# Performance work log

Measured on AMD Instinct MI355X. Metric: run time of the kernel, lower is better.

## Reference

```python
import jax, jax.numpy as jnp
import numpy as np

# TensorProductConvLayer (DiffDock-style): gather -> edge-MLP-weighted fully
# connected tensor product (lmax=1 irreps) -> scatter-mean.
# in/out irreps: ns x0e + nv x1o + nv x1e + ns x0o ; sh irreps: 1x0e + 1x1o
NS, NV = 16, 4
N_NODES, N_EDGES = 8000, 160000
EDGE_FEAT = 3 * NS                      # 48
IRREPS_DIM = 2 * NS + 6 * NV            # 56
# per-path weight block sizes (fully-connected 'uvw' paths, mul2 = 1):
# [A:0e*0e->0e, B:1o*1o->0e, A:0e*1o->1o, B:1o*0e->1o, C:1e*1o->1o,
#  B:1o*1o->1e, C:1e*0e->1e, D:0o*1o->1e, C:1e*1o->0o, D:0o*0e->0o]
PATH_SIZES = [NS*NS, NV*NS, NS*NV, NV*NV, NV*NV, NV*NV, NV*NV, NS*NV, NV*NS, NS*NS]
W_NUMEL = sum(PATH_SIZES)               # 832
# component-normalized CG factors: 1x1->0 uses delta/sqrt(3); 1x1->1 uses eps/sqrt(2)
INV_SQRT3 = float(1.0 / np.sqrt(3.0))
INV_SQRT2 = float(1.0 / np.sqrt(2.0))
# element path normalization: 1/sqrt(total fan-in mul per output irrep)
A_SCAL = float(1.0 / np.sqrt(NS + NV))      # 0e / 0o outputs
A_VEC = float(1.0 / np.sqrt(NS + 2 * NV))   # 1o / 1e outputs


def setup_inputs() -> dict:
    key = jax.random.key(0)
    ks = jax.random.split(key, 6)
    node_attr = jax.random.normal(ks[0], (N_NODES, IRREPS_DIM), jnp.float32)
    edge_index = jax.random.randint(ks[1], (2, N_EDGES), 0, N_NODES)
    edge_attr = jax.random.normal(ks[2], (N_EDGES, EDGE_FEAT), jnp.float32)
    edge_sh = jax.random.normal(ks[3], (N_EDGES, 4), jnp.float32)
    s = float(1.0 / np.sqrt(EDGE_FEAT))
    fc_w1 = jax.random.normal(ks[4], (EDGE_FEAT, EDGE_FEAT), jnp.float32) * s
    fc_b1 = jnp.zeros((EDGE_FEAT,), jnp.float32)
    fc_w2 = jax.random.normal(ks[5], (EDGE_FEAT, W_NUMEL), jnp.float32) * s
    fc_b2 = jnp.zeros((W_NUMEL,), jnp.float32)
    return dict(node_attr=node_attr, edge_attr=edge_attr, edge_sh=edge_sh,
                fc_w1=fc_w1, fc_b1=fc_b1, fc_w2=fc_w2, fc_b2=fc_b2,
                edge_index=edge_index)


def _split_weights(w):
    outs, off = [], 0
    for sz in PATH_SIZES:
        outs.append(w[:, off:off + sz])
        off += sz
    return outs


def _tp_conv(node_attr, edge_attr, edge_sh, fc_w1, fc_b1, fc_w2, fc_b2, src, dst):
    # edge MLP -> per-edge tensor-product weights [E, 832]
    h = jax.nn.relu(edge_attr @ fc_w1 + fc_b1)
    w = h @ fc_w2 + fc_b2
    wA0, wB0, wA1, wB1, wC1, wB1e, wC1e, wD1e, wC0o, wD0o = _split_weights(w)

    x = node_attr[dst]                         # gather [E, 56]
    x0e = x[:, :NS]
    x1o = x[:, NS:NS + 3 * NV].reshape(-1, NV, 3)
    x1e = x[:, NS + 3 * NV:NS + 6 * NV].reshape(-1, NV, 3)
    x0o = x[:, NS + 6 * NV:]
    s0 = edge_sh[:, 0]
    s1 = edge_sh[:, 1:4]

    # ---- 0e output [E, ns]
    o0e = jnp.einsum('eu,euv->ev', x0e, wA0.reshape(-1, NS, NS)) * s0[:, None]
    dot_b = jnp.einsum('eui,ei->eu', x1o, s1) * INV_SQRT3   # 1o x 1o -> 0e
    o0e = (o0e + jnp.einsum('eu,euv->ev', dot_b, wB0.reshape(-1, NV, NS))) * A_SCAL

    # ---- 1o output [E, nv, 3]
    o1o = jnp.einsum('eu,euv->ev', x0e, wA1.reshape(-1, NS, NV))[:, :, None] * s1[:, None, :]
    o1o = o1o + jnp.einsum('eui,euv->evi', x1o, wB1.reshape(-1, NV, NV)) * s0[:, None, None]
    cr_e = jnp.cross(x1e, s1[:, None, :]) * INV_SQRT2       # 1e x 1o -> 1o
    o1o = (o1o + jnp.einsum('eui,euv->evi', cr_e, wC1.reshape(-1, NV, NV))) * A_VEC

    # ---- 1e output [E, nv, 3]
    cr_o = jnp.cross(x1o, s1[:, None, :]) * INV_SQRT2       # 1o x 1o -> 1e
    o1e = jnp.einsum('eui,euv->evi', cr_o, wB1e.reshape(-1, NV, NV))
    o1e = o1e + jnp.einsum('eui,euv->evi', x1e, wC1e.reshape(-1, NV, NV)) * s0[:, None, None]
    o1e = (o1e + jnp.einsum('eu,euv->ev', x0o, wD1e.reshape(-1, NS, NV))[:, :, None] * s1[:, None, :]) * A_VEC

    # ---- 0o output [E, ns]
    dot_c = jnp.einsum('eui,ei->eu', x1e, s1) * INV_SQRT3   # 1e x 1o -> 0o
    o0o = jnp.einsum('eu,euv->ev', dot_c, wC0o.reshape(-1, NV, NS))
    o0o = (o0o + jnp.einsum('eu,euv->ev', x0o, wD0o.reshape(-1, NS, NS)) * s0[:, None]) * A_SCAL

    tp = jnp.concatenate([o0e, o1o.reshape(-1, 3 * NV), o1e.reshape(-1, 3 * NV), o0o], axis=-1)

    # scatter-mean over source nodes
    summed = jax.ops.segment_sum(tp, src, num_segments=N_NODES)
    counts = jax.ops.segment_sum(jnp.ones((tp.shape[0],), tp.dtype), src, num_segments=N_NODES)
    return summed / jnp.maximum(counts, 1.0)[:, None]


def reference(node_attr, edge_attr, edge_sh, fc_w1, fc_b1, fc_w2, fc_b2, edge_index):
    src, dst = edge_index[0], edge_index[1]
    return _tp_conv(node_attr, edge_attr, edge_sh, fc_w1, fc_b1, fc_w2, fc_b2, src, dst)
```

## Files before the change

### kernel.cpp

```cpp
#include <hip/hip_runtime.h>
#include <hip/hip_fp16.h>

#define IRR    56
#define EF     48
#define WN     832
#define NEDGE  160000
#define NNODE  8000
#define NT     256
#define TE2    64
#define NTASK  (NEDGE / TE2)
#define GRID   512

#define INV_SQRT3 0.5773502691896258f
#define INV_SQRT2 0.7071067811865476f
#define A_SCAL    0.22360679774997896f
#define A_VEC     0.20412414523193154f

typedef __bf16 bf16x8 __attribute__((ext_vector_type(8)));
typedef float  f32x4  __attribute__((ext_vector_type(4)));
typedef unsigned short u16x8 __attribute__((ext_vector_type(8)));
typedef unsigned short u16x4 __attribute__((ext_vector_type(4)));

__device__ __forceinline__ unsigned short f2bf(float f) {
    unsigned int u = __builtin_bit_cast(unsigned int, f);
    u += 0x7FFFu + ((u >> 16) & 1u);
    return (unsigned short)(u >> 16);
}
__device__ __forceinline__ unsigned short f2h(float f) {
    __half h = __float2half(f);
    return __builtin_bit_cast(unsigned short, h);
}
__device__ __forceinline__ float h2f(unsigned short u) {
    __half h = __builtin_bit_cast(__half, u);
    return __half2float(h);
}

__global__ void k_setup(const float* __restrict__ w1, const float* __restrict__ b1,
                        const float* __restrict__ w2, const float* __restrict__ b2,
                        unsigned short* __restrict__ W1T, unsigned short* __restrict__ W2L,
                        const int* __restrict__ edge_index, int* __restrict__ hist)
{
    int o = blockIdx.x * 256 + threadIdx.x;
    if (o < 52 * 2 * 64 * 8) {
        int i = o >> 10;
        int rem = o & 1023;
        int f = rem >> 9;
        int rem2 = rem & 511;
        int l = rem2 >> 3, j = rem2 & 7;
        int mm = l & 15, qq = l >> 4;
        int k = f * 32 + qq * 8 + j;
        int n = i * 16 + mm;
        float v = (k < EF) ? w2[k * WN + n] : ((k == EF) ? b2[n] : 0.f);
        W2L[o] = f2bf(v);
    }
    if (o < EF * EF) { int k = o / EF, n = o - k * EF; W1T[n * 64 + k] = f2bf(w1[o]); }
    if (o < EF * 16) { int n = o >> 4, kk = EF + (o & 15); W1T[n * 64 + kk] = (kk == EF) ? f2bf(b1[n]) : (unsigned short)0; }
    if (o < NEDGE) atomicAdd(&hist[edge_index[o]], 1);
}

__global__ __launch_bounds__(NT, 2) void tp_fused(
    const float* __restrict__ node_attr,
    const float* __restrict__ edge_attr,
    const float* __restrict__ edge_sh,
    const int*   __restrict__ edge_index,
    const int*   __restrict__ hist,
    const unsigned short* __restrict__ W1T,
    const unsigned short* __restrict__ W2L,
    float* __restrict__ out)
{
    __shared__ __align__(16) unsigned short sW2[26 * 1024];
    __shared__ __align__(16) unsigned char  UGH[TE2 * 56 * 4];
    __shared__ __align__(16) unsigned char  UFO[TE2 * 60 * 2];
    __shared__ float sS1[TE2][4];
    __shared__ int   sSrc[TE2], sDst[TE2];
    __shared__ float sInv[TE2];

    float*          sG   = (float*)UGH;
    unsigned short* sH   = (unsigned short*)UGH;
    unsigned short* sF16 = (unsigned short*)UFO;
    float*          sO   = (float*)UFO;

    const int tid    = threadIdx.x;
    const int lane   = tid & 63;
    const int wv     = tid >> 6;
    const int m      = lane & 15;
    const int quad   = lane >> 4;
    const int em     = wv * 16 + m;
    const int flavor = blockIdx.x & 1;
    const int bid2   = blockIdx.x >> 1;

    {
        const uint4* src = (const uint4*)(W2L + (size_t)flavor * 26 * 1024);
        uint4* dst = (uint4*)sW2;
        #pragma unroll
        for (int it = 0; it < 13; it++) dst[it * NT + tid] = src[it * NT + tid];
    }

    for (int task = bid2; task < NTASK; task += 256) {
        const int e0 = task * TE2;
        __syncthreads();
        if (tid < TE2)            sSrc[tid]       = edge_index[e0 + tid];
        else if (tid < 2 * TE2)   sDst[tid - TE2] = edge_index[NEDGE + e0 + tid - TE2];
        __syncthreads();

        {
            const float* nrow = node_attr + (size_t)sDst[em] * IRR;
            float* g = sG + em * 56;
            #pragma unroll
            for (int t = 0; t < 3; t++) {
                int c = quad + t * 4;
                *(float4*)(g + c * 4) = *(const float4*)(nrow + c * 4);
            }
            if (quad < 2) { int c = 12 + quad; *(float4*)(g + c * 4) = *(const float4*)(nrow + c * 4); }
        }
        if (tid >= 128 && tid < 128 + TE2) {
            int e = tid - 128;
            sInv[e] = 1.0f / fmaxf((float)hist[sSrc[e]], 1.0f);
        }
        __syncthreads();

        if (quad == 0) {
            const float* x = sG + em * 56;
            float4 sh4 = *(const float4*)&edge_sh[(size_t)(e0 + em) * 4];
            const float s0 = sh4.x, sx = sh4.y, sy = sh4.z, sz = sh4.w;
            unsigned short* F = sF16 + em * 60;
            const float c0S = s0 * A_SCAL;
            const float c0V = s0 * A_VEC;
            const float cD3 = INV_SQRT3 * A_SCAL;
            const float cC2 = INV_SQRT2 * A_VEC;
            if (flavor == 0) {
                #pragma unroll
                for (int u = 0; u < 16; u++) {
                    float x0e = x[u];
                    F[u]      = f2h(x0e * c0S);
                    F[20 + u] = f2h(x0e * A_VEC);
                }
                #pragma unroll
                for (int u = 0; u < 4; u++) {
                    float a0 = x[16 + u*3], a1 = x[16 + u*3 + 1], a2 = x[16 + u*3 + 2];
                    float b0 = x[28 + u*3], b1 = x[28 + u*3 + 1], b2 = x[28 + u*3 + 2];
                    F[16 + u] = f2h((a0*sx + a1*sy + a2*sz) * cD3);
                    F[36 + u*3 + 0] = f2h(a0 * c0V);
                    F[36 + u*3 + 1] = f2h(a1 * c0V);
                    F[36 + u*3 + 2] = f2h(a2 * c0V);
                    F[48 + u*3 + 0] = f2h((b1*sz - b2*sy) * cC2);
                    F[48 + u*3 + 1] = f2h((b2*sx - b0*sz) * cC2);
                    F[48 + u*3 + 2] = f2h((b0*sy - b1*sx) * cC2);
                }
            } else {
                #pragma unroll
                for (int u = 0; u < 4; u++) {
                    float a0 = x[16 + u*3], a1 = x[16 + u*3 + 1], a2 = x[16 + u*3 + 2];
                    float b0 = x[28 + u*3], b1 = x[28 + u*3 + 1], b2 = x[28 + u*3 + 2];
                    F[u*3 + 0]      = f2h((a1*sz - a2*sy) * cC2);
                    F[u*3 + 1]      = f2h((a2*sx - a0*sz) * cC2);
                    F[u*3 + 2]      = f2h((a0*sy - a1*sx) * cC2);
                    F[12 + u*3 + 0] = f2h(b0 * c0V);
                    F[12 + u*3 + 1] = f2h(b1 * c0V);
                    F[12 + u*3 + 2] = f2h(b2 * c0V);
                    F[40 + u]       = f2h((b0*sx + b1*sy + b2*sz) * cD3);
                }
                #pragma unroll
                for (int u = 0; u < 16; u++) {
                    float x0o = x[40 + u];
                    F[24 + u] = f2h(x0o * A_VEC);
                    F[44 + u] = f2h(x0o * c0S);
                }
            }
            sS1[em][0] = sx; sS1[em][1] = sy; sS1[em][2] = sz;
        }
        __syncthreads();

        {
            const float* arow = edge_attr + (size_t)(e0 + em) * EF;
            float av0[8], av1[8];
            {
                float4 p0 = *(const float4*)(arow + quad * 8);
                float4 p1 = *(const float4*)(arow + quad * 8 + 4);
                av0[0]=p0.x; av0[1]=p0.y; av0[2]=p0.z; av0[3]=p0.w;
                av0[4]=p1.x; av0[5]=p1.y; av0[6]=p1.z; av0[7]=p1.w;
            }
            if (quad < 2) {
                float4 p0 = *(const float4*)(arow + 32 + quad * 8);
                float4 p1 = *(const float4*)(arow + 32 + quad * 8 + 4);
                av1[0]=p0.x; av1[1]=p0.y; av1[2]=p0.z; av1[3]=p0.w;
                av1[4]=p1.x; av1[5]=p1.y; av1[6]=p1.z; av1[7]=p1.w;
            } else {
                #pragma unroll
                for (int j = 0; j < 8; j++) av1[j] = 0.f;
                if (quad == 2) av1[0] = 1.f;
            }
            u16x8 ub0, ub1;
            #pragma unroll
            for (int j = 0; j < 8; j++) { ub0[j] = f2bf(av0[j]); ub1[j] = f2bf(av1[j]); }
            bf16x8 hb0 = __builtin_bit_cast(bf16x8, ub0);
            bf16x8 hb1 = __builtin_bit_cast(bf16x8, ub1);

            #pragma unroll
            for (int nth = 0; nth < 3; nth++) {
                bf16x8 a0 = __builtin_bit_cast(bf16x8, *(const u16x8*)&W1T[(nth*16 + m)*64 + quad*8]);
                bf16x8 a1 = __builtin_bit_cast(bf16x8, *(const u16x8*)&W1T[(nth*16 + m)*64 + 32 + quad*8]);
                f32x4 c = {0.f, 0.f, 0.f, 0.f};
                c = __builtin_amdgcn_mfma_f32_16x16x32_bf16(a0, hb0, c, 0, 0, 0);
                c = __builtin_amdgcn_mfma_f32_16x16x32_bf16(a1, hb1, c, 0, 0, 0);
                u16x4 hp;
                #pragma unroll
                for (int r = 0; r < 4; r++) hp[r] = f2bf(fmaxf(c[r], 0.f));
                *(u16x4*)&sH[em * 72 + nth*16 + quad*4] = hp;
            }
            if (quad == 3) {
                u16x4 b = {0x3F80, 0, 0, 0}, z = {0, 0, 0, 0};
                *(u16x4*)&sH[em * 72 + 48] = b;
                *(u16x4*)&sH[em * 72 + 52] = z;
                *(u16x4*)&sH[em * 72 + 56] = z;
                *(u16x4*)&sH[em * 72 + 60] = z;
            }
        }
        __syncthreads();

        bf16x8 HB0 = __builtin_bit_cast(bf16x8, *(const u16x8*)&sH[em * 72 + quad*8]);
        bf16x8 HB1 = __builtin_bit_cast(bf16x8, *(const u16x8*)&sH[em * 72 + 32 + quad*8]);

        const unsigned short* Fp = sF16 + em * 60;
        const float s1x = sS1[em][0], s1y = sS1[em][1], s1z = sS1[em][2];

        if (flavor == 0) {
            float oe[4] = {0.f,0.f,0.f,0.f};
            float sA[4] = {0.f,0.f,0.f,0.f};
            float t1[12] = {0.f,0.f,0.f,0.f,0.f,0.f,0.f,0.f,0.f,0.f,0.f,0.f};
            #pragma unroll
            for (int i = 0; i < 26; i++) {
                u16x8 Af = *(const u16x8*)&sW2[i * 1024 + lane * 8];
                u16x8 Bf = *(const u16x8*)&sW2[i * 1024 + 512 + lane * 8];
                f32x4 c = {0.f,0.f,0.f,0.f};
                c = __builtin_amdgcn_mfma_f32_16x16x32_bf16(__builtin_bit_cast(bf16x8, Af), HB0, c, 0, 0, 0);
                c = __builtin_amdgcn_mfma_f32_16x16x32_bf16(__builtin_bit_cast(bf16x8, Bf), HB1, c, 0, 0, 0);
                if (i < 20) {
                    float f = h2f(Fp[i]);
                    #pragma unroll
                    for (int r = 0; r < 4; r++) oe[r] += f * c[r];
                } else if (i < 24) {
                    float f = h2f(Fp[20 + (i - 20)*4 + quad]);
                    #pragma unroll
                    for (int r = 0; r < 4; r++) sA[r] += f * c[r];
                } else {
                    int u = (i - 24)*4 + quad;
                    #pragma unroll
                    for (int i3 = 0; i3 < 3; i3++) {
                        float f = h2f(Fp[36 + u*3 + i3]);
                        #pragma unroll
                        for (int r = 0; r < 4; r++) t1[i3*4 + r] += f * c[r];
                    }
                }
            }
            #pragma unroll
            for (int r = 0; r < 4; r++) {
                sA[r] += __shfl_xor(sA[r], 16, 64);  sA[r] += __shfl_xor(sA[r], 32, 64);
            }
            #pragma unroll
            for (int i = 0; i < 12; i++) {
                t1[i] += __shfl_xor(t1[i], 16, 64);  t1[i] += __shfl_xor(t1[i], 32, 64);
            }
            __syncthreads();
            float4 v0; v0.x = oe[0]; v0.y = oe[1]; v0.z = oe[2]; v0.w = oe[3];
            *(float4*)&sO[em * 28 + quad*4] = v0;
            if (quad == 0) {
                #pragma unroll
                for (int r = 0; r < 4; r++) {
                    sO[em * 28 + 16 + r*3 + 0] = sA[r] * s1x + t1[0*4 + r];
                    sO[em * 28 + 16 + r*3 + 1] = sA[r] * s1y + t1[1*4 + r];
                    sO[em * 28 + 16 + r*3 + 2] = sA[r] * s1z + t1[2*4 + r];
                }
            }
        } else {
            float sD[4] = {0.f,0.f,0.f,0.f};
            float t1[12] = {0.f,0.f,0.f,0.f,0.f,0.f,0.f,0.f,0.f,0.f,0.f,0.f};
            float oo[4] = {0.f,0.f,0.f,0.f};
            #pragma unroll
            for (int i = 0; i < 26; i++) {
                u16x8 Af = *(const u16x8*)&sW2[i * 1024 + lane * 8];
                u16x8 Bf = *(const u16x8*)&sW2[i * 1024 + 512 + lane * 8];
                f32x4 c = {0.f,0.f,0.f,0.f};
                c = __builtin_amdgcn_mfma_f32_16x16x32_bf16(__builtin_bit_cast(bf16x8, Af), HB0, c, 0, 0, 0);
                c = __builtin_amdgcn_mfma_f32_16x16x32_bf16(__builtin_bit_cast(bf16x8, Bf), HB1, c, 0, 0, 0);
                if (i < 2) {
                    int j = i*4 + quad;
                    #pragma unroll
                    for (int i3 = 0; i3 < 3; i3++) {
                        float f = h2f(Fp[j*3 + i3]);
                        #pragma unroll
                        for (int r = 0; r < 4; r++) t1[i3*4 + r] += f * c[r];
                    }
                } else if (i < 6) {
                    float f = h2f(Fp[24 + (i - 2)*4 + quad]);
                    #pragma unroll
                    for (int r = 0; r < 4; r++) sD[r] += f * c[r];
                } else {
                    float f = h2f(Fp[40 + (i - 6)]);
                    #pragma unroll
                    for (int r = 0; r < 4; r++) oo[r] += f * c[r];
                }
            }
            #pragma unroll
            for (int r = 0; r < 4; r++) {
                sD[r] += __shfl_xor(sD[r], 16, 64);  sD[r] += __shfl_xor(sD[r], 32, 64);
            }
            #pragma unroll
            for (int i = 0; i < 12; i++) {
                t1[i] += __shfl_xor(t1[i], 16, 64);  t1[i] += __shfl_xor(t1[i], 32, 64);
            }
            __syncthreads();
            float4 v1; v1.x = oo[0]; v1.y = oo[1]; v1.z = oo[2]; v1.w = oo[3];
            *(float4*)&sO[em * 28 + 12 + quad*4] = v1;
            if (quad == 0) {
                #pragma unroll
                for (int r = 0; r < 4; r++) {
                    sO[em * 28 + r*3 + 0] = sD[r] * s1x + t1[0*4 + r];
                    sO[em * 28 + r*3 + 1] = sD[r] * s1y + t1[1*4 + r];
                    sO[em * 28 + r*3 + 2] = sD[r] * s1z + t1[2*4 + r];
                }
            }
        }
        __syncthreads();

        #pragma unroll
        for (int it = 0; it < 7; it++) {
            int idx = it * NT + tid;
            int e = idx / 28, ch = idx - e * 28;
            unsafeAtomicAdd(&out[(size_t)sSrc[e] * IRR + flavor * 28 + ch],
                            sO[e * 28 + ch] * sInv[e]);
        }
    }
}

extern "C" void kernel_launch(void* const* d_in, const int* in_sizes, int n_in,
                              void* d_out, int out_size, void* d_ws, size_t ws_size,
                              hipStream_t stream) {
    const float* node_attr  = (const float*)d_in[0];
    const float* edge_attr  = (const float*)d_in[1];
    const float* edge_sh    = (const float*)d_in[2];
    const float* fc_w1      = (const float*)d_in[3];
    const float* fc_b1      = (const float*)d_in[4];
    const float* fc_w2      = (const float*)d_in[5];
    const float* fc_b2      = (const float*)d_in[6];
    const int*   edge_index = (const int*)d_in[7];

    int* hist = (int*)d_ws;
    unsigned short* W1T = (unsigned short*)(hist + NNODE);
    unsigned short* W2L = W1T + EF * 64;

    hipMemsetAsync(hist, 0, NNODE * sizeof(int), stream);
    hipMemsetAsync(d_out, 0, (size_t)out_size * sizeof(float), stream);

    k_setup<<<(NEDGE + 255) / 256, 256, 0, stream>>>(
        fc_w1, fc_b1, fc_w2, fc_b2, W1T, W2L, edge_index, hist);

    tp_fused<<<GRID, NT, 0, stream>>>(node_attr, edge_attr, edge_sh, edge_index,
                                      hist, W1T, W2L, (float*)d_out);
}
```

Before: 177.9 us.

## Drop persistent LDS-resident W2 loop for one-block-per-tile grid with global weight reads

Replaces the persistent kernel, which staged the second-layer weights into about 52KB of shared memory per block, with a grid of one block per 64-edge tile per flavor. The weights are now read straight from global memory and served from cache, and launch bounds rise to 4 blocks per CU. The per-edge factor computation is spread across all four quads and stored as fp32 instead of fp16. Several barriers per tile are removed. The aim is more occupancy and less synchronization, at the cost of repeated global or L2 weight fetches per MFMA and more blocks to launch.

```diff
diff --git a/kernel.cpp b/kernel.cpp
--- a/kernel.cpp
+++ b/kernel.cpp
@@ -9,7 +9,7 @@
 #define NT     256
 #define TE2    64
 #define NTASK  (NEDGE / TE2)
-#define GRID   512
+#define GRID   (2 * NTASK)
 
 #define INV_SQRT3 0.5773502691896258f
 #define INV_SQRT2 0.7071067811865476f
@@ -25,14 +25,6 @@
     unsigned int u = __builtin_bit_cast(unsigned int, f);
     u += 0x7FFFu + ((u >> 16) & 1u);
     return (unsigned short)(u >> 16);
-}
-__device__ __forceinline__ unsigned short f2h(float f) {
-    __half h = __float2half(f);
-    return __builtin_bit_cast(unsigned short, h);
-}
-__device__ __forceinline__ float h2f(unsigned short u) {
-    __half h = __builtin_bit_cast(__half, u);
-    return __half2float(h);
 }
 
 __global__ void k_setup(const float* __restrict__ w1, const float* __restrict__ b1,
@@ -58,7 +50,7 @@
     if (o < NEDGE) atomicAdd(&hist[edge_index[o]], 1);
 }
 
-__global__ __launch_bounds__(NT, 2) void tp_fused(
+__global__ __launch_bounds__(NT, 4) void tp_fused(
     const float* __restrict__ node_attr,
     const float* __restrict__ edge_attr,
     const float* __restrict__ edge_sh,
@@ -68,17 +60,14 @@
     const unsigned short* __restrict__ W2L,
     float* __restrict__ out)
 {
-    __shared__ __align__(16) unsigned short sW2[26 * 1024];
-    __shared__ __align__(16) unsigned char  UGH[TE2 * 56 * 4];
-    __shared__ __align__(16) unsigned char  UFO[TE2 * 60 * 2];
-    __shared__ float sS1[TE2][4];
+    __shared__ __align__(16) unsigned char UGH[TE2 * 56 * 4];
+    __shared__ __align__(16) float sF[TE2 * 61];
+    __shared__ __align__(16) float sO[TE2 * 28];
     __shared__ int   sSrc[TE2], sDst[TE2];
     __shared__ float sInv[TE2];
 
-    float*          sG   = (float*)UGH;
-    unsigned short* sH   = (unsigned short*)UGH;
-    unsigned short* sF16 = (unsigned short*)UFO;
-    float*          sO   = (float*)UFO;
+    float*          sG = (float*)UGH;
+    unsigned short* sH = (unsigned short*)UGH;
 
     const int tid    = threadIdx.x;
     const int lane   = tid & 63;
@@ -87,249 +76,239 @@
     const int quad   = lane >> 4;
     const int em     = wv * 16 + m;
     const int flavor = blockIdx.x & 1;
-    const int bid2   = blockIdx.x >> 1;
+    const int e0     = (blockIdx.x >> 1) * TE2;
+
+    if (tid < TE2)            sSrc[tid]       = edge_index[e0 + tid];
+    else if (tid < 2 * TE2)   sDst[tid - TE2] = edge_index[NEDGE + e0 + tid - TE2];
+    __syncthreads();
 
     {
-        const uint4* src = (const uint4*)(W2L + (size_t)flavor * 26 * 1024);
-        uint4* dst = (uint4*)sW2;
-        #pragma unroll
-        for (int it = 0; it < 13; it++) dst[it * NT + tid] = src[it * NT + tid];
-    }
-
-    for (int task = bid2; task < NTASK; task += 256) {
-        const int e0 = task * TE2;
-        __syncthreads();
-        if (tid < TE2)            sSrc[tid]       = edge_index[e0 + tid];
-        else if (tid < 2 * TE2)   sDst[tid - TE2] = edge_index[NEDGE + e0 + tid - TE2];
-        __syncthreads();
-
+        const float* nrow = node_attr + (size_t)sDst[em] * IRR;
+        float* g = sG + em * 56;
+        #pragma unroll
+        for (int t = 0; t < 3; t++) {
+            int c = quad + t * 4;
+            *(float4*)(g + c * 4) = *(const float4*)(nrow + c * 4);
+        }
+        if (quad < 2) { int c = 12 + quad; *(float4*)(g + c * 4) = *(const float4*)(nrow + c * 4); }
+    }
+    if (tid >= 128 && tid < 128 + TE2) {
+        int e = tid - 128;
+        sInv[e] = 1.0f / fmaxf((float)hist[sSrc[e]], 1.0f);
+    }
+
+    float4 sh4 = *(const float4*)&edge_sh[(size_t)(e0 + em) * 4];
+    const float s0 = sh4.x, sx = sh4.y, sy = sh4.z, sz = sh4.w;
+
+    {
+        const float* x = sG + em * 56;
+        float* F = sF + em * 61;
+        const float c0S = s0 * A_SCAL;
+        const float c0V = s0 * A_VEC;
+        const float cD3 = INV_SQRT3 * A_SCAL;
+        const float cC2 = INV_SQRT2 * A_VEC;
+        if (flavor == 0) {
+            #pragma unroll
+            for (int t = 0; t < 4; t++) {
+                int u = quad * 4 + t;
+                float x0e = x[u];
+                F[u]      = x0e * c0S;
+                F[20 + u] = x0e * A_VEC;
+            }
+            {
+                int u = quad;
+                float a0 = x[16 + u*3], a1 = x[16 + u*3 + 1], a2 = x[16 + u*3 + 2];
+                float b0 = x[28 + u*3], b1 = x[28 + u*3 + 1], b2 = x[28 + u*3 + 2];
+                F[16 + u] = (a0*sx + a1*sy + a2*sz) * cD3;
+                F[36 + u*3 + 0] = a0 * c0V;
+                F[36 + u*3 + 1] = a1 * c0V;
+                F[36 + u*3 + 2] = a2 * c0V;
+                F[48 + u*3 + 0] = (b1*sz - b2*sy) * cC2;
+                F[48 + u*3 + 1] = (b2*sx - b0*sz) * cC2;
+                F[48 + u*3 + 2] = (b0*sy - b1*sx) * cC2;
+            }
+        } else {
+            {
+                int u = quad;
+                float a0 = x[16 + u*3], a1 = x[16 + u*3 + 1], a2 = x[16 + u*3 + 2];
+                float b0 = x[28 + u*3], b1 = x[28 + u*3 + 1], b2 = x[28 + u*3 + 2];
+                F[u*3 + 0]      = (a1*sz - a2*sy) * cC2;
+                F[u*3 + 1]      = (a2*sx - a0*sz) * cC2;
+                F[u*3 + 2]      = (a0*sy - a1*sx) * cC2;
+                F[12 + u*3 + 0] = b0 * c0V;
+                F[12 + u*3 + 1] = b1 * c0V;
+                F[12 + u*3 + 2] = b2 * c0V;
+                F[40 + u]       = (b0*sx + b1*sy + b2*sz) * cD3;
+            }
+            #pragma unroll
+            for (int t = 0; t < 4; t++) {
+                int u = quad * 4 + t;
+                float x0o = x[40 + u];
+                F[24 + u] = x0o * A_VEC;
+                F[44 + u] = x0o * c0S;
+            }
+        }
+    }
+
+    bf16x8 hb0, hb1;
+    {
+        const float* arow = edge_attr + (size_t)(e0 + em) * EF;
+        float av0[8], av1[8];
         {
-            const float* nrow = node_attr + (size_t)sDst[em] * IRR;
-            float* g = sG + em * 56;
-            #pragma unroll
-            for (int t = 0; t < 3; t++) {
-                int c = quad + t * 4;
-                *(float4*)(g + c * 4) = *(const float4*)(nrow + c * 4);
-            }
-            if (quad < 2) { int c = 12 + quad; *(float4*)(g + c * 4) = *(const float4*)(nrow + c * 4); }
-        }
-        if (tid >= 128 && tid < 128 + TE2) {
-            int e = tid - 128;
-            sInv[e] = 1.0f / fmaxf((float)hist[sSrc[e]], 1.0f);
-        }
-        __syncthreads();
-
+            float4 p0 = *(const float4*)(arow + quad * 8);
+            float4 p1 = *(const float4*)(arow + quad * 8 + 4);
+            av0[0]=p0.x; av0[1]=p0.y; av0[2]=p0.z; av0[3]=p0.w;
+            av0[4]=p1.x; av0[5]=p1.y; av0[6]=p1.z; av0[7]=p1.w;
+        }
+        if (quad < 2) {
+            float4 p0 = *(const float4*)(arow + 32 + quad * 8);
+            float4 p1 = *(const float4*)(arow + 32 + quad * 8 + 4);
+            av1[0]=p0.x; av1[1]=p0.y; av1[2]=p0.z; av1[3]=p0.w;
+            av1[4]=p1.x; av1[5]=p1.y; av1[6]=p1.z; av1[7]=p1.w;
+        } else {
+            #pragma unroll
+            for (int j = 0; j < 8; j++) av1[j] = 0.f;
+            if (quad == 2) av1[0] = 1.f;
+        }
+        u16x8 ub0, ub1;
+        #pragma unroll
+        for (int j = 0; j < 8; j++) { ub0[j] = f2bf(av0[j]); ub1[j] = f2bf(av1[j]); }
+        hb0 = __builtin_bit_cast(bf16x8, ub0);
+        hb1 = __builtin_bit_cast(bf16x8, ub1);
+    }
+
+    __syncthreads();
+
+    #pragma unroll
+    for (int nth = 0; nth < 3; nth++) {
+        bf16x8 a0 = __builtin_bit_cast(bf16x8, *(const u16x8*)&W1T[(nth*16 + m)*64 + quad*8]);
+        bf16x8 a1 = __builtin_bit_cast(bf16x8, *(const u16x8*)&W1T[(nth*16 + m)*64 + 32 + quad*8]);
+        f32x4 c = {0.f, 0.f, 0.f, 0.f};
+        c = __builtin_amdgcn_mfma_f32_16x16x32_bf16(a0, hb0, c, 0, 0, 0);
+        c = __builtin_amdgcn_mfma_f32_16x16x32_bf16(a1, hb1, c, 0, 0, 0);
+        u16x4 hp;
+        #pragma unroll
+        for (int r = 0; r < 4; r++) hp[r] = f2bf(fmaxf(c[r], 0.f));
+        *(u16x4*)&sH[em * 72 + nth*16 + quad*4] = hp;
+    }
+    if (quad == 3) {
+        u16x4 b = {0x3F80, 0, 0, 0}, z = {0, 0, 0, 0};
+        *(u16x4*)&sH[em * 72 + 48] = b;
+        *(u16x4*)&sH[em * 72 + 52] = z;
+        *(u16x4*)&sH[em * 72 + 56] = z;
+        *(u16x4*)&sH[em * 72 + 60] = z;
+    }
+
+    bf16x8 HB0 = __builtin_bit_cast(bf16x8, *(const u16x8*)&sH[em * 72 + quad*8]);
+    bf16x8 HB1 = __builtin_bit_cast(bf16x8, *(const u16x8*)&sH[em * 72 + 32 + quad*8]);
+
+    const float* Fp = sF + em * 61;
+    const unsigned short* Wt = W2L + (size_t)flavor * 26 * 1024;
+
+    if (flavor == 0) {
+        float oe[4] = {0.f,0.f,0.f,0.f};
+        float sA[4] = {0.f,0.f,0.f,0.f};
+        float t1[12] = {0.f,0.f,0.f,0.f,0.f,0.f,0.f,0.f,0.f,0.f,0.f,0.f};
+        #pragma unroll
+        for (int i = 0; i < 26; i++) {
+            u16x8 Af = *(const u16x8*)&Wt[i * 1024 + lane * 8];
+            u16x8 Bf = *(const u16x8*)&Wt[i * 1024 + 512 + lane * 8];
+            f32x4 c = {0.f,0.f,0.f,0.f};
+            c = __builtin_amdgcn_mfma_f32_16x16x32_bf16(__builtin_bit_cast(bf16x8, Af), HB0, c, 0, 0, 0);
+            c = __builtin_amdgcn_mfma_f32_16x16x32_bf16(__builtin_bit_cast(bf16x8, Bf), HB1, c, 0, 0, 0);
+            if (i < 20) {
+                float f = Fp[i];
+                #pragma unroll
+                for (int r = 0; r < 4; r++) oe[r] += f * c[r];
+            } else if (i < 24) {
+                float f = Fp[20 + (i - 20)*4 + quad];
+                #pragma unroll
+                for (int r = 0; r < 4; r++) sA[r] += f * c[r];
+            } else {
+                int u = (i - 24)*4 + quad;
+                #pragma unroll
+                for (int i3 = 0; i3 < 3; i3++) {
+                    float f = Fp[36 + u*3 + i3];
+                    #pragma unroll
+                    for (int r = 0; r < 4; r++) t1[i3*4 + r] += f * c[r];
+                }
+            }
+        }
+        #pragma unroll
+        for (int r = 0; r < 4; r++) {
+            sA[r] += __shfl_xor(sA[r], 16, 64);  sA[r] += __shfl_xor(sA[r], 32, 64);
+        }
+        #pragma unroll
+        for (int i = 0; i < 12; i++) {
+            t1[i] += __shfl_xor(t1[i], 16, 64);  t1[i] += __shfl_xor(t1[i], 32, 64);
+        }
+        float4 v0; v0.x = oe[0]; v0.y = oe[1]; v0.z = oe[2]; v0.w = oe[3];
+        *(float4*)&sO[em * 28 + quad*4] = v0;
         if (quad == 0) {
-            const float* x = sG + em * 56;
-            float4 sh4 = *(const float4*)&edge_sh[(size_t)(e0 + em) * 4];
-            const float s0 = sh4.x, sx = sh4.y, sy = sh4.z, sz = sh4.w;
-            unsigned short* F = sF16 + em * 60;
-            const float c0S = s0 * A_SCAL;
-            const float c0V = s0 * A_VEC;
-            const float cD3 = INV_SQRT3 * A_SCAL;
-            const float cC2 = INV_SQRT2 * A_VEC;
-            if (flavor == 0) {
-                #pragma unroll
-                for (int u = 0; u < 16; u++) {
-                    float x0e = x[u];
-                    F[u]      = f2h(x0e * c0S);
-                    F[20 + u] = f2h(x0e * A_VEC);
+            #pragma unroll
+            for (int r = 0; r < 4; r++) {
+                sO[em * 28 + 16 + r*3 + 0] = sA[r] * sx + t1[0*4 + r];
+                sO[em * 28 + 16 + r*3 + 1] = sA[r] * sy + t1[1*4 + r];
+                sO[em * 28 + 16 + r*3 + 2] = sA[r] * sz + t1[2*4 + r];
+            }
+        }
+    } else {
+        float sD[4] = {0.f,0.f,0.f,0.f};
+        float t1[12] = {0.f,0.f,0.f,0.f,0.f,0.f,0.f,0.f,0.f,0.f,0.f,0.f};
+        float oo[4] = {0.f,0.f,0.f,0.f};
+        #pragma unroll
+        for (int i = 0; i < 26; i++) {
+            u16x8 Af = *(const u16x8*)&Wt[i * 1024 + lane * 8];
+            u16x8 Bf = *(const u16x8*)&Wt[i * 1024 + 512 + lane * 8];
+            f32x4 c = {0.f,0.f,0.f,0.f};
+            c = __builtin_amdgcn_mfma_f32_16x16x32_bf16(__builtin_bit_cast(bf16x8, Af), HB0, c, 0, 0, 0);
+            c = __builtin_amdgcn_mfma_f32_16x16x32_bf16(__builtin_bit_cast(bf16x8, Bf), HB1, c, 0, 0, 0);
+            if (i < 2) {
+                int j = i*4 + quad;
+                #pragma unroll
+                for (int i3 = 0; i3 < 3; i3++) {
+                    float f = Fp[j*3 + i3];
+                    #pragma unroll
+                    for (int r = 0; r < 4; r++) t1[i3*4 + r] += f * c[r];
                 }
-                #pragma unroll
-                for (int u = 0; u < 4; u++) {
-                    float a0 = x[16 + u*3], a1 = x[16 + u*3 + 1], a2 = x[16 + u*3 + 2];
-                    float b0 = x[28 + u*3], b1 = x[28 + u*3 + 1], b2 = x[28 + u*3 + 2];
-                    F[16 + u] = f2h((a0*sx + a1*sy + a2*sz) * cD3);
-                    F[36 + u*3 + 0] = f2h(a0 * c0V);
-                    F[36 + u*3 + 1] = f2h(a1 * c0V);
-                    F[36 + u*3 + 2] = f2h(a2 * c0V);
-                    F[48 + u*3 + 0] = f2h((b1*sz - b2*sy) * cC2);
-                    F[48 + u*3 + 1] = f2h((b2*sx - b0*sz) * cC2);
-                    F[48 + u*3 + 2] = f2h((b0*sy - b1*sx) * cC2);
-                }
+            } else if (i < 6) {
+                float f = Fp[24 + (i - 2)*4 + quad];
+                #pragma unroll
+                for (int r = 0; r < 4; r++) sD[r] += f * c[r];
             } else {
-                #pragma unroll
-                for (int u = 0; u < 4; u++) {
-                    float a0 = x[16 + u*3], a1 = x[16 + u*3 + 1], a2 = x[16 + u*3 + 2];
-                    float b0 = x[28 + u*3], b1 = x[28 + u*3 + 1], b2 = x[28 + u*3 + 2];
-                    F[u*3 + 0]      = f2h((a1*sz - a2*sy) * cC2);
-                    F[u*3 + 1]      = f2h((a2*sx - a0*sz) * cC2);
-                    F[u*3 + 2]      = f2h((a0*sy - a1*sx) * cC2);
-                    F[12 + u*3 + 0] = f2h(b0 * c0V);
-                    F[12 + u*3 + 1] = f2h(b1 * c0V);
-                    F[12 + u*3 + 2] = f2h(b2 * c0V);
-                    F[40 + u]       = f2h((b0*sx + b1*sy + b2*sz) * cD3);
-                }
-                #pragma unroll
-                for (int u = 0; u < 16; u++) {
-                    float x0o = x[40 + u];
-                    F[24 + u] = f2h(x0o * A_VEC);
-                    F[44 + u] = f2h(x0o * c0S);
-                }
-            }
-            sS1[em][0] = sx; sS1[em][1] = sy; sS1[em][2] = sz;
-        }
-        __syncthreads();
-
-        {
-            const float* arow = edge_attr + (size_t)(e0 + em) * EF;
-            float av0[8], av1[8];
-            {
-                float4 p0 = *(const float4*)(arow + quad * 8);
-                float4 p1 = *(const float4*)(arow + quad * 8 + 4);
-                av0[0]=p0.x; av0[1]=p0.y; av0[2]=p0.z; av0[3]=p0.w;
-                av0[4]=p1.x; av0[5]=p1.y; av0[6]=p1.z; av0[7]=p1.w;
-            }
-            if (quad < 2) {
-                float4 p0 = *(const float4*)(arow + 32 + quad * 8);
-                float4 p1 = *(const float4*)(arow + 32 + quad * 8 + 4);
-                av1[0]=p0.x; av1[1]=p0.y; av1[2]=p0.z; av1[3]=p0.w;
-                av1[4]=p1.x; av1[5]=p1.y; av1[6]=p1.z; av1[7]=p1.w;
-            } else {
-                #pragma unroll
-                for (int j = 0; j < 8; j++) av1[j] = 0.f;
-                if (quad == 2) av1[0] = 1.f;
-            }
-            u16x8 ub0, ub1;
-            #pragma unroll
-            for (int j = 0; j < 8; j++) { ub0[j] = f2bf(av0[j]); ub1[j] = f2bf(av1[j]); }
-            bf16x8 hb0 = __builtin_bit_cast(bf16x8, ub0);
-            bf16x8 hb1 = __builtin_bit_cast(bf16x8, ub1);
-
-            #pragma unroll
-            for (int nth = 0; nth < 3; nth++) {
-                bf16x8 a0 = __builtin_bit_cast(bf16x8, *(const u16x8*)&W1T[(nth*16 + m)*64 + quad*8]);
-                bf16x8 a1 = __builtin_bit_cast(bf16x8, *(const u16x8*)&W1T[(nth*16 + m)*64 + 32 + quad*8]);
-                f32x4 c = {0.f, 0.f, 0.f, 0.f};
-                c = __builtin_amdgcn_mfma_f32_16x16x32_bf16(a0, hb0, c, 0, 0, 0);
-                c = __builtin_amdgcn_mfma_f32_16x16x32_bf16(a1, hb1, c, 0, 0, 0);
-                u16x4 hp;
-                #pragma unroll
-                for (int r = 0; r < 4; r++) hp[r] = f2bf(fmaxf(c[r], 0.f));
-                *(u16x4*)&sH[em * 72 + nth*16 + quad*4] = hp;
-            }
-            if (quad == 3) {
-                u16x4 b = {0x3F80, 0, 0, 0}, z = {0, 0, 0, 0};
-                *(u16x4*)&sH[em * 72 + 48] = b;
-                *(u16x4*)&sH[em * 72 + 52] = z;
-                *(u16x4*)&sH[em * 72 + 56] = z;
-                *(u16x4*)&sH[em * 72 + 60] = z;
-            }
-        }
-        __syncthreads();
-
-        bf16x8 HB0 = __builtin_bit_cast(bf16x8, *(const u16x8*)&sH[em * 72 + quad*8]);
-        bf16x8 HB1 = __builtin_bit_cast(bf16x8, *(const u16x8*)&sH[em * 72 + 32 + quad*8]);
-
-        const unsigned short* Fp = sF16 + em * 60;
-        const float s1x = sS1[em][0], s1y = sS1[em][1], s1z = sS1[em][2];
-
-        if (flavor == 0) {
-            float oe[4] = {0.f,0.f,0.f,0.f};
-            float sA[4] = {0.f,0.f,0.f,0.f};
-            float t1[12] = {0.f,0.f,0.f,0.f,0.f,0.f,0.f,0.f,0.f,0.f,0.f,0.f};
-            #pragma unroll
-            for (int i = 0; i < 26; i++) {
-                u16x8 Af = *(const u16x8*)&sW2[i * 1024 + lane * 8];
-                u16x8 Bf = *(const u16x8*)&sW2[i * 1024 + 512 + lane * 8];
-                f32x4 c = {0.f,0.f,0.f,0.f};
-                c = __builtin_amdgcn_mfma_f32_16x16x32_bf16(__builtin_bit_cast(bf16x8, Af), HB0, c, 0, 0, 0);
-                c = __builtin_amdgcn_mfma_f32_16x16x32_bf16(__builtin_bit_cast(bf16x8, Bf), HB1, c, 0, 0, 0);
-                if (i < 20) {
-                    float f = h2f(Fp[i]);
-                    #pragma unroll
-                    for (int r = 0; r < 4; r++) oe[r] += f * c[r];
-                } else if (i < 24) {
-                    float f = h2f(Fp[20 + (i - 20)*4 + quad]);
-                    #pragma unroll
-                    for (int r = 0; r < 4; r++) sA[r] += f * c[r];
-                } else {
-                    int u = (i - 24)*4 + quad;
-                    #pragma unroll
-                    for (int i3 = 0; i3 < 3; i3++) {
-                        float f = h2f(Fp[36 + u*3 + i3]);
-                        #pragma unroll
-                        for (int r = 0; r < 4; r++) t1[i3*4 + r] += f * c[r];
-                    }
-                }
-            }
+                float f = Fp[40 + (i - 6)];
+                #pragma unroll
+                for (int r = 0; r < 4; r++) oo[r] += f * c[r];
+            }
+        }
+        #pragma unroll
+        for (int r = 0; r < 4; r++) {
+            sD[r] += __shfl_xor(sD[r], 16, 64);  sD[r] += __shfl_xor(sD[r], 32, 64);
+        }
+        #pragma unroll
+        for (int i = 0; i < 12; i++) {
+            t1[i] += __shfl_xor(t1[i], 16, 64);  t1[i] += __shfl_xor(t1[i], 32, 64);
+        }
+        float4 v1; v1.x = oo[0]; v1.y = oo[1]; v1.z = oo[2]; v1.w = oo[3];
+        *(float4*)&sO[em * 28 + 12 + quad*4] = v1;
+        if (quad == 0) {
             #pragma unroll
             for (int r = 0; r < 4; r++) {
-                sA[r] += __shfl_xor(sA[r], 16, 64);  sA[r] += __shfl_xor(sA[r], 32, 64);
-            }
-            #pragma unroll
-            for (int i = 0; i < 12; i++) {
-                t1[i] += __shfl_xor(t1[i], 16, 64);  t1[i] += __shfl_xor(t1[i], 32, 64);
-            }
-            __syncthreads();
-            float4 v0; v0.x = oe[0]; v0.y = oe[1]; v0.z = oe[2]; v0.w = oe[3];
-            *(float4*)&sO[em * 28 + quad*4] = v0;
-            if (quad == 0) {
-                #pragma unroll
-                for (int r = 0; r < 4; r++) {
-                    sO[em * 28 + 16 + r*3 + 0] = sA[r] * s1x + t1[0*4 + r];
-                    sO[em * 28 + 16 + r*3 + 1] = sA[r] * s1y + t1[1*4 + r];
-                    sO[em * 28 + 16 + r*3 + 2] = sA[r] * s1z + t1[2*4 + r];
-                }
-            }
-        } else {
-            float sD[4] = {0.f,0.f,0.f,0.f};
-            float t1[12] = {0.f,0.f,0.f,0.f,0.f,0.f,0.f,0.f,0.f,0.f,0.f,0.f};
-            float oo[4] = {0.f,0.f,0.f,0.f};
-            #pragma unroll
-            for (int i = 0; i < 26; i++) {
-                u16x8 Af = *(const u16x8*)&sW2[i * 1024 + lane * 8];
-                u16x8 Bf = *(const u16x8*)&sW2[i * 1024 + 512 + lane * 8];
-                f32x4 c = {0.f,0.f,0.f,0.f};
-                c = __builtin_amdgcn_mfma_f32_16x16x32_bf16(__builtin_bit_cast(bf16x8, Af), HB0, c, 0, 0, 0);
-                c = __builtin_amdgcn_mfma_f32_16x16x32_bf16(__builtin_bit_cast(bf16x8, Bf), HB1, c, 0, 0, 0);
-                if (i < 2) {
-                    int j = i*4 + quad;
-                    #pragma unroll
-                    for (int i3 = 0; i3 < 3; i3++) {
-                        float f = h2f(Fp[j*3 + i3]);
-                        #pragma unroll
-                        for (int r = 0; r < 4; r++) t1[i3*4 + r] += f * c[r];
-                    }
-                } else if (i < 6) {
-                    float f = h2f(Fp[24 + (i - 2)*4 + quad]);
-                    #pragma unroll
-                    for (int r = 0; r < 4; r++) sD[r] += f * c[r];
-                } else {
-                    float f = h2f(Fp[40 + (i - 6)]);
-                    #pragma unroll
-                    for (int r = 0; r < 4; r++) oo[r] += f * c[r];
-                }
-            }
-            #pragma unroll
-            for (int r = 0; r < 4; r++) {
-                sD[r] += __shfl_xor(sD[r], 16, 64);  sD[r] += __shfl_xor(sD[r], 32, 64);
-            }
-            #pragma unroll
-            for (int i = 0; i < 12; i++) {
-                t1[i] += __shfl_xor(t1[i], 16, 64);  t1[i] += __shfl_xor(t1[i], 32, 64);
-            }
-            __syncthreads();
-            float4 v1; v1.x = oo[0]; v1.y = oo[1]; v1.z = oo[2]; v1.w = oo[3];
-            *(float4*)&sO[em * 28 + 12 + quad*4] = v1;
-            if (quad == 0) {
-                #pragma unroll
-                for (int r = 0; r < 4; r++) {
-                    sO[em * 28 + r*3 + 0] = sD[r] * s1x + t1[0*4 + r];
-                    sO[em * 28 + r*3 + 1] = sD[r] * s1y + t1[1*4 + r];
-                    sO[em * 28 + r*3 + 2] = sD[r] * s1z + t1[2*4 + r];
-                }
-            }
-        }
-        __syncthreads();
-
-        #pragma unroll
-        for (int it = 0; it < 7; it++) {
-            int idx = it * NT + tid;
-            int e = idx / 28, ch = idx - e * 28;
-            unsafeAtomicAdd(&out[(size_t)sSrc[e] * IRR + flavor * 28 + ch],
-                            sO[e * 28 + ch] * sInv[e]);
-        }
+                sO[em * 28 + r*3 + 0] = sD[r] * sx + t1[0*4 + r];
+                sO[em * 28 + r*3 + 1] = sD[r] * sy + t1[1*4 + r];
+                sO[em * 28 + r*3 + 2] = sD[r] * sz + t1[2*4 + r];
+            }
+        }
+    }
+
+    __syncthreads();
+
+    #pragma unroll
+    for (int it = 0; it < 7; it++) {
+        int idx = it * NT + tid;
+        int e = idx / 28, ch = idx - e * 28;
+        unsafeAtomicAdd(&out[(size_t)sSrc[e] * IRR + flavor * 28 + ch],
+                        sO[e * 28 + ch] * sInv[e]);
     }
 }
 
```

Result: no change. 176.8 us (-0.6%).

## Remove block barriers by making each wave own its edges and atomics

Applied to the files above, without the earlier changes.

The per-task edge loop is restructured so every wave processes its own 16 edges end to end. Each wave loads its own src/dst indices, inverse counts and spherical harmonics into registers, spreads the feature-prep work across all four quads, and keeps W1 MFMA fragments in registers for the whole kernel. Results are atomically added straight from registers instead of being staged in shared memory, which removes all __syncthreads inside the loop. The setup kernel's W2 relayout is rewritten to read w2 with coalesced loads. In exchange, the atomic adds are scattered and less coalesced, and the extra long-lived registers raise register pressure.

```diff
diff --git a/kernel.cpp b/kernel.cpp
--- a/kernel.cpp
+++ b/kernel.cpp
@@ -9,7 +9,8 @@
 #define NT     256
 #define TE2    64
 #define NTASK  (NEDGE / TE2)
-#define GRID   512
+#define NBLK2  256
+#define GRID   (2 * NBLK2)
 
 #define INV_SQRT3 0.5773502691896258f
 #define INV_SQRT2 0.7071067811865476f
@@ -41,17 +42,14 @@
                         const int* __restrict__ edge_index, int* __restrict__ hist)
 {
     int o = blockIdx.x * 256 + threadIdx.x;
-    if (o < 52 * 2 * 64 * 8) {
-        int i = o >> 10;
-        int rem = o & 1023;
-        int f = rem >> 9;
-        int rem2 = rem & 511;
-        int l = rem2 >> 3, j = rem2 & 7;
-        int mm = l & 15, qq = l >> 4;
-        int k = f * 32 + qq * 8 + j;
-        int n = i * 16 + mm;
+    if (o < 64 * 832) {
+        int k = o / 832;
+        int n = o - k * 832;
         float v = (k < EF) ? w2[k * WN + n] : ((k == EF) ? b2[n] : 0.f);
-        W2L[o] = f2bf(v);
+        int i = n >> 4, mm = n & 15;
+        int f = k >> 5, q = (k >> 3) & 3, j = k & 7;
+        int o2 = (((i * 2 + f) * 64) + (q * 16 + mm)) * 8 + j;
+        W2L[o2] = f2bf(v);
     }
     if (o < EF * EF) { int k = o / EF, n = o - k * EF; W1T[n * 64 + k] = f2bf(w1[o]); }
     if (o < EF * 16) { int n = o >> 4, kk = EF + (o & 15); W1T[n * 64 + kk] = (kk == EF) ? f2bf(b1[n]) : (unsigned short)0; }
@@ -70,15 +68,7 @@
 {
     __shared__ __align__(16) unsigned short sW2[26 * 1024];
     __shared__ __align__(16) unsigned char  UGH[TE2 * 56 * 4];
-    __shared__ __align__(16) unsigned char  UFO[TE2 * 60 * 2];
-    __shared__ float sS1[TE2][4];
-    __shared__ int   sSrc[TE2], sDst[TE2];
-    __shared__ float sInv[TE2];
-
-    float*          sG   = (float*)UGH;
-    unsigned short* sH   = (unsigned short*)UGH;
-    unsigned short* sF16 = (unsigned short*)UFO;
-    float*          sO   = (float*)UFO;
+    __shared__ __align__(16) unsigned short sF[TE2 * 61];
 
     const int tid    = threadIdx.x;
     const int lane   = tid & 63;
@@ -89,54 +79,89 @@
     const int flavor = blockIdx.x & 1;
     const int bid2   = blockIdx.x >> 1;
 
+    float*          sGrow = (float*)UGH + em * 56;
+    unsigned short* sHrow = (unsigned short*)UGH + wv * 1792 + m * 72;
+    unsigned short* sFrow = sF + em * 61;
+
     {
-        const uint4* src = (const uint4*)(W2L + (size_t)flavor * 26 * 1024);
-        uint4* dst = (uint4*)sW2;
+        const uint4* srcp = (const uint4*)(W2L + (size_t)flavor * 26 * 1024);
+        uint4* dstp = (uint4*)sW2;
         #pragma unroll
-        for (int it = 0; it < 13; it++) dst[it * NT + tid] = src[it * NT + tid];
+        for (int it = 0; it < 13; it++) dstp[it * NT + tid] = srcp[it * NT + tid];
     }
 
-    for (int task = bid2; task < NTASK; task += 256) {
+    bf16x8 a00 = __builtin_bit_cast(bf16x8, *(const u16x8*)&W1T[( 0 + m) * 64 + quad * 8]);
+    bf16x8 a01 = __builtin_bit_cast(bf16x8, *(const u16x8*)&W1T[( 0 + m) * 64 + 32 + quad * 8]);
+    bf16x8 a10 = __builtin_bit_cast(bf16x8, *(const u16x8*)&W1T[(16 + m) * 64 + quad * 8]);
+    bf16x8 a11 = __builtin_bit_cast(bf16x8, *(const u16x8*)&W1T[(16 + m) * 64 + 32 + quad * 8]);
+    bf16x8 a20 = __builtin_bit_cast(bf16x8, *(const u16x8*)&W1T[(32 + m) * 64 + quad * 8]);
+    bf16x8 a21 = __builtin_bit_cast(bf16x8, *(const u16x8*)&W1T[(32 + m) * 64 + 32 + quad * 8]);
+
+    __syncthreads();
+
+    for (int task = bid2; task < NTASK; task += NBLK2) {
         const int e0 = task * TE2;
-        __syncthreads();
-        if (tid < TE2)            sSrc[tid]       = edge_index[e0 + tid];
-        else if (tid < 2 * TE2)   sDst[tid - TE2] = edge_index[NEDGE + e0 + tid - TE2];
-        __syncthreads();
+
+        const int   srcn = edge_index[e0 + em];
+        const int   dstn = edge_index[NEDGE + e0 + em];
+        const float inv  = 1.0f / fmaxf((float)hist[srcn], 1.0f);
+        float4 sh4 = *(const float4*)&edge_sh[(size_t)(e0 + em) * 4];
+        const float s0 = sh4.x, sx = sh4.y, sy = sh4.z, sz = sh4.w;
 
         {
-            const float* nrow = node_attr + (size_t)sDst[em] * IRR;
-            float* g = sG + em * 56;
+            const float* nrow = node_attr + (size_t)dstn * IRR;
             #pragma unroll
             for (int t = 0; t < 3; t++) {
                 int c = quad + t * 4;
-                *(float4*)(g + c * 4) = *(const float4*)(nrow + c * 4);
-            }
-            if (quad < 2) { int c = 12 + quad; *(float4*)(g + c * 4) = *(const float4*)(nrow + c * 4); }
-        }
-        if (tid >= 128 && tid < 128 + TE2) {
-            int e = tid - 128;
-            sInv[e] = 1.0f / fmaxf((float)hist[sSrc[e]], 1.0f);
-        }
-        __syncthreads();
-
-        if (quad == 0) {
-            const float* x = sG + em * 56;
-            float4 sh4 = *(const float4*)&edge_sh[(size_t)(e0 + em) * 4];
-            const float s0 = sh4.x, sx = sh4.y, sy = sh4.z, sz = sh4.w;
-            unsigned short* F = sF16 + em * 60;
+                *(float4*)(sGrow + c * 4) = *(const float4*)(nrow + c * 4);
+            }
+            if (quad < 2) { int c = 12 + quad; *(float4*)(sGrow + c * 4) = *(const float4*)(nrow + c * 4); }
+        }
+
+        bf16x8 hb0, hb1;
+        {
+            const float* arow = edge_attr + (size_t)(e0 + em) * EF;
+            float av0[8], av1[8];
+            {
+                float4 p0 = *(const float4*)(arow + quad * 8);
+                float4 p1 = *(const float4*)(arow + quad * 8 + 4);
+                av0[0]=p0.x; av0[1]=p0.y; av0[2]=p0.z; av0[3]=p0.w;
+                av0[4]=p1.x; av0[5]=p1.y; av0[6]=p1.z; av0[7]=p1.w;
+            }
+            if (quad < 2) {
+                float4 p0 = *(const float4*)(arow + 32 + quad * 8);
+                float4 p1 = *(const float4*)(arow + 32 + quad * 8 + 4);
+                av1[0]=p0.x; av1[1]=p0.y; av1[2]=p0.z; av1[3]=p0.w;
+                av1[4]=p1.x; av1[5]=p1.y; av1[6]=p1.z; av1[7]=p1.w;
+            } else {
+                #pragma unroll
+                for (int j = 0; j < 8; j++) av1[j] = 0.f;
+                if (quad == 2) av1[0] = 1.f;
+            }
+            u16x8 ub0, ub1;
+            #pragma unroll
+            for (int j = 0; j < 8; j++) { ub0[j] = f2bf(av0[j]); ub1[j] = f2bf(av1[j]); }
+            hb0 = __builtin_bit_cast(bf16x8, ub0);
+            hb1 = __builtin_bit_cast(bf16x8, ub1);
+        }
+
+        {
+            const float* x = sGrow;
             const float c0S = s0 * A_SCAL;
             const float c0V = s0 * A_VEC;
             const float cD3 = INV_SQRT3 * A_SCAL;
             const float cC2 = INV_SQRT2 * A_VEC;
+            unsigned short* F = sFrow;
             if (flavor == 0) {
                 #pragma unroll
-                for (int u = 0; u < 16; u++) {
+                for (int t = 0; t < 4; t++) {
+                    int u = quad * 4 + t;
                     float x0e = x[u];
                     F[u]      = f2h(x0e * c0S);
                     F[20 + u] = f2h(x0e * A_VEC);
                 }
-                #pragma unroll
-                for (int u = 0; u < 4; u++) {
+                {
+                    int u = quad;
                     float a0 = x[16 + u*3], a1 = x[16 + u*3 + 1], a2 = x[16 + u*3 + 2];
                     float b0 = x[28 + u*3], b1 = x[28 + u*3 + 1], b2 = x[28 + u*3 + 2];
                     F[16 + u] = f2h((a0*sx + a1*sy + a2*sz) * cD3);
@@ -148,8 +173,8 @@
                     F[48 + u*3 + 2] = f2h((b0*sy - b1*sx) * cC2);
                 }
             } else {
-                #pragma unroll
-                for (int u = 0; u < 4; u++) {
+                {
+                    int u = quad;
                     float a0 = x[16 + u*3], a1 = x[16 + u*3 + 1], a2 = x[16 + u*3 + 2];
                     float b0 = x[28 + u*3], b1 = x[28 + u*3 + 1], b2 = x[28 + u*3 + 2];
                     F[u*3 + 0]      = f2h((a1*sz - a2*sy) * cC2);
@@ -161,68 +186,46 @@
                     F[40 + u]       = f2h((b0*sx + b1*sy + b2*sz) * cD3);
                 }
                 #pragma unroll
-                for (int u = 0; u < 16; u++) {
+                for (int t = 0; t < 4; t++) {
+                    int u = quad * 4 + t;
                     float x0o = x[40 + u];
                     F[24 + u] = f2h(x0o * A_VEC);
                     F[44 + u] = f2h(x0o * c0S);
                 }
             }
-            sS1[em][0] = sx; sS1[em][1] = sy; sS1[em][2] = sz;
-        }
-        __syncthreads();
+        }
 
         {
-            const float* arow = edge_attr + (size_t)(e0 + em) * EF;
-            float av0[8], av1[8];
-            {
-                float4 p0 = *(const float4*)(arow + quad * 8);
-                float4 p1 = *(const float4*)(arow + quad * 8 + 4);
-                av0[0]=p0.x; av0[1]=p0.y; av0[2]=p0.z; av0[3]=p0.w;
-                av0[4]=p1.x; av0[5]=p1.y; av0[6]=p1.z; av0[7]=p1.w;
-            }
-            if (quad < 2) {
-                float4 p0 = *(const float4*)(arow + 32 + quad * 8);
-                float4 p1 = *(const float4*)(arow + 32 + quad * 8 + 4);
-                av1[0]=p0.x; av1[1]=p0.y; av1[2]=p0.z; av1[3]=p0.w;
-                av1[4]=p1.x; av1[5]=p1.y; av1[6]=p1.z; av1[7]=p1.w;
-            } else {
-                #pragma unroll
-                for (int j = 0; j < 8; j++) av1[j] = 0.f;
-                if (quad == 2) av1[0] = 1.f;
-            }
-            u16x8 ub0, ub1;
-            #pragma unroll
-            for (int j = 0; j < 8; j++) { ub0[j] = f2bf(av0[j]); ub1[j] = f2bf(av1[j]); }
-            bf16x8 hb0 = __builtin_bit_cast(bf16x8, ub0);
-            bf16x8 hb1 = __builtin_bit_cast(bf16x8, ub1);
-
-            #pragma unroll
-            for (int nth = 0; nth < 3; nth++) {
-                bf16x8 a0 = __builtin_bit_cast(bf16x8, *(const u16x8*)&W1T[(nth*16 + m)*64 + quad*8]);
-                bf16x8 a1 = __builtin_bit_cast(bf16x8, *(const u16x8*)&W1T[(nth*16 + m)*64 + 32 + quad*8]);
-                f32x4 c = {0.f, 0.f, 0.f, 0.f};
-                c = __builtin_amdgcn_mfma_f32_16x16x32_bf16(a0, hb0, c, 0, 0, 0);
-                c = __builtin_amdgcn_mfma_f32_16x16x32_bf16(a1, hb1, c, 0, 0, 0);
-                u16x4 hp;
-                #pragma unroll
-                for (int r = 0; r < 4; r++) hp[r] = f2bf(fmaxf(c[r], 0.f));
-                *(u16x4*)&sH[em * 72 + nth*16 + quad*4] = hp;
-            }
+            f32x4 c0 = {0.f,0.f,0.f,0.f}, c1 = {0.f,0.f,0.f,0.f}, c2 = {0.f,0.f,0.f,0.f};
+            c0 = __builtin_amdgcn_mfma_f32_16x16x32_bf16(a00, hb0, c0, 0, 0, 0);
+            c0 = __builtin_amdgcn_mfma_f32_16x16x32_bf16(a01, hb1, c0, 0, 0, 0);
+            c1 = __builtin_amdgcn_mfma_f32_16x16x32_bf16(a10, hb0, c1, 0, 0, 0);
+            c1 = __builtin_amdgcn_mfma_f32_16x16x32_bf16(a11, hb1, c1, 0, 0, 0);
+            c2 = __builtin_amdgcn_mfma_f32_16x16x32_bf16(a20, hb0, c2, 0, 0, 0);
+            c2 = __builtin_amdgcn_mfma_f32_16x16x32_bf16(a21, hb1, c2, 0, 0, 0);
+            u16x4 h0, h1, h2;
+            #pragma unroll
+            for (int r = 0; r < 4; r++) {
+                h0[r] = f2bf(fmaxf(c0[r], 0.f));
+                h1[r] = f2bf(fmaxf(c1[r], 0.f));
+                h2[r] = f2bf(fmaxf(c2[r], 0.f));
+            }
+            *(u16x4*)&sHrow[ 0 + quad*4] = h0;
+            *(u16x4*)&sHrow[16 + quad*4] = h1;
+            *(u16x4*)&sHrow[32 + quad*4] = h2;
             if (quad == 3) {
                 u16x4 b = {0x3F80, 0, 0, 0}, z = {0, 0, 0, 0};
-                *(u16x4*)&sH[em * 72 + 48] = b;
-                *(u16x4*)&sH[em * 72 + 52] = z;
-                *(u16x4*)&sH[em * 72 + 56] = z;
-                *(u16x4*)&sH[em * 72 + 60] = z;
-            }
-        }
-        __syncthreads();
-
-        bf16x8 HB0 = __builtin_bit_cast(bf16x8, *(const u16x8*)&sH[em * 72 + quad*8]);
-        bf16x8 HB1 = __builtin_bit_cast(bf16x8, *(const u16x8*)&sH[em * 72 + 32 + quad*8]);
-
-        const unsigned short* Fp = sF16 + em * 60;
-        const float s1x = sS1[em][0], s1y = sS1[em][1], s1z = sS1[em][2];
+                *(u16x4*)&sHrow[48] = b;
+                *(u16x4*)&sHrow[52] = z;
+                *(u16x4*)&sHrow[56] = z;
+                *(u16x4*)&sHrow[60] = z;
+            }
+        }
+
+        bf16x8 HB0 = __builtin_bit_cast(bf16x8, *(const u16x8*)&sHrow[quad*8]);
+        bf16x8 HB1 = __builtin_bit_cast(bf16x8, *(const u16x8*)&sHrow[32 + quad*8]);
+        float* orow = out + (size_t)srcn * IRR;
+        const unsigned short* Fp = sFrow;
 
         if (flavor == 0) {
             float oe[4] = {0.f,0.f,0.f,0.f};
@@ -261,16 +264,14 @@
             for (int i = 0; i < 12; i++) {
                 t1[i] += __shfl_xor(t1[i], 16, 64);  t1[i] += __shfl_xor(t1[i], 32, 64);
             }
-            __syncthreads();
-            float4 v0; v0.x = oe[0]; v0.y = oe[1]; v0.z = oe[2]; v0.w = oe[3];
-            *(float4*)&sO[em * 28 + quad*4] = v0;
-            if (quad == 0) {
-                #pragma unroll
-                for (int r = 0; r < 4; r++) {
-                    sO[em * 28 + 16 + r*3 + 0] = sA[r] * s1x + t1[0*4 + r];
-                    sO[em * 28 + 16 + r*3 + 1] = sA[r] * s1y + t1[1*4 + r];
-                    sO[em * 28 + 16 + r*3 + 2] = sA[r] * s1z + t1[2*4 + r];
-                }
+            #pragma unroll
+            for (int r = 0; r < 4; r++)
+                unsafeAtomicAdd(&orow[quad*4 + r], oe[r] * inv);
+            #pragma unroll
+            for (int q = 0; q < 4; q++) if (quad == q) {
+                unsafeAtomicAdd(&orow[16 + q*3 + 0], (sA[q]*sx + t1[0*4 + q]) * inv);
+                unsafeAtomicAdd(&orow[16 + q*3 + 1], (sA[q]*sy + t1[1*4 + q]) * inv);
+                unsafeAtomicAdd(&orow[16 + q*3 + 2], (sA[q]*sz + t1[2*4 + q]) * inv);
             }
         } else {
             float sD[4] = {0.f,0.f,0.f,0.f};
@@ -309,26 +310,15 @@
             for (int i = 0; i < 12; i++) {
                 t1[i] += __shfl_xor(t1[i], 16, 64);  t1[i] += __shfl_xor(t1[i], 32, 64);
             }
-            __syncthreads();
-            float4 v1; v1.x = oo[0]; v1.y = oo[1]; v1.z = oo[2]; v1.w = oo[3];
-            *(float4*)&sO[em * 28 + 12 + quad*4] = v1;
-            if (quad == 0) {
-                #pragma unroll
-                for (int r = 0; r < 4; r++) {
-                    sO[em * 28 + r*3 + 0] = sD[r] * s1x + t1[0*4 + r];
-                    sO[em * 28 + r*3 + 1] = sD[r] * s1y + t1[1*4 + r];
-                    sO[em * 28 + r*3 + 2] = sD[r] * s1z + t1[2*4 + r];
-                }
-            }
-        }
-        __syncthreads();
-
-        #pragma unroll
-        for (int it = 0; it < 7; it++) {
-            int idx = it * NT + tid;
-            int e = idx / 28, ch = idx - e * 28;
-            unsafeAtomicAdd(&out[(size_t)sSrc[e] * IRR + flavor * 28 + ch],
-                            sO[e * 28 + ch] * sInv[e]);
+            #pragma unroll
+            for (int r = 0; r < 4; r++)
+                unsafeAtomicAdd(&orow[40 + quad*4 + r], oo[r] * inv);
+            #pragma unroll
+            for (int q = 0; q < 4; q++) if (quad == q) {
+                unsafeAtomicAdd(&orow[28 + q*3 + 0], (sD[q]*sx + t1[0*4 + q]) * inv);
+                unsafeAtomicAdd(&orow[28 + q*3 + 1], (sD[q]*sy + t1[1*4 + q]) * inv);
+                unsafeAtomicAdd(&orow[28 + q*3 + 2], (sD[q]*sz + t1[2*4 + q]) * inv);
+            }
         }
     }
 }
```

New measurement: 415.3 us. +133.4%, slower.
